# Kernel optimization log

Measured on AMD Instinct MI355X. Metric: run time of the kernel, lower is better.

## Reference

```python
import jax, jax.numpy as jnp
import numpy as np

NUM_NODES = 100000
NUM_EDGES = 1600000
NUM_GRAPHS = 64
IN_DIM = 128
HID = 128
OUT_DIM = 256
NUM_LAYERS = 5
BN_EPS = 1e-5


def _bn(t, gamma, beta):
    # BatchNorm1d forward with batch statistics (biased variance), as in train mode
    m = jnp.mean(t, axis=0)
    v = jnp.var(t, axis=0)
    return gamma * (t - m) * jax.lax.rsqrt(v + BN_EPS) + beta


def setup_inputs() -> dict:
    key = jax.random.key(0)
    ks = jax.random.split(key, 16)
    x = jax.random.normal(ks[0], (NUM_NODES, IN_DIM), dtype=jnp.float32)
    edge_index = jax.random.randint(ks[1], (2, NUM_EDGES), 0, NUM_NODES, dtype=jnp.int64)
    batch = jnp.sort(jax.random.randint(ks[2], (NUM_NODES,), 0, NUM_GRAPHS, dtype=jnp.int64))
    s1 = 1.0 / np.sqrt(IN_DIM)
    s2 = 1.0 / np.sqrt(HID)
    # stacked per-layer GIN MLP params: Linear(HID,HID) -> BN -> ReLU -> Linear(HID,HID)
    w1 = jax.random.normal(ks[3], (NUM_LAYERS, HID, HID), dtype=jnp.float32) * s1
    b1 = jnp.zeros((NUM_LAYERS, HID), dtype=jnp.float32)
    gamma1 = jnp.ones((NUM_LAYERS, HID), dtype=jnp.float32)
    beta1 = jnp.zeros((NUM_LAYERS, HID), dtype=jnp.float32)
    w2 = jax.random.normal(ks[4], (NUM_LAYERS, HID, HID), dtype=jnp.float32) * s2
    b2 = jnp.zeros((NUM_LAYERS, HID), dtype=jnp.float32)
    # outer per-layer BatchNorm after each GINConv
    gamma_bn = jnp.ones((NUM_LAYERS, HID), dtype=jnp.float32)
    beta_bn = jnp.zeros((NUM_LAYERS, HID), dtype=jnp.float32)
    # output projection Linear(HID, OUT_DIM)
    wp = jax.random.normal(ks[5], (HID, OUT_DIM), dtype=jnp.float32) * s2
    bp = jnp.zeros((OUT_DIM,), dtype=jnp.float32)
    return {"x": x, "edge_index": edge_index, "batch": batch,
            "w1": w1, "b1": b1, "gamma1": gamma1, "beta1": beta1,
            "w2": w2, "b2": b2, "gamma_bn": gamma_bn, "beta_bn": beta_bn,
            "wp": wp, "bp": bp}


def reference(x, edge_index, batch, w1, b1, gamma1, beta1, w2, b2, gamma_bn, beta_bn, wp, bp):
    src, dst = edge_index[0], edge_index[1]
    h = x
    for i in range(NUM_LAYERS):
        # GINConv, eps=0: mlp((1+eps)*h + sum_{j in N(i)} h_j)
        agg = jax.ops.segment_sum(h[src], dst, num_segments=NUM_NODES)
        z = h + agg
        t = _bn(z @ w1[i] + b1[i], gamma1[i], beta1[i])
        t = jax.nn.relu(t)
        t = t @ w2[i] + b2[i]
        # outer BatchNorm + ReLU (dropout p handled as identity in eval)
        t = jax.nn.relu(_bn(t, gamma_bn[i], beta_bn[i]))
        h = h + t  # residual (dims always match)
    node_emb = h
    # global mean pool per graph
    sums = jax.ops.segment_sum(h, batch, num_segments=NUM_GRAPHS)
    counts = jax.ops.segment_sum(jnp.ones((NUM_NODES,), dtype=h.dtype), batch, num_segments=NUM_GRAPHS)
    pooled = sums / jnp.maximum(counts, 1.0)[:, None]
    graph_emb = pooled @ wp + bp
    return graph_emb, node_emb
```

## Files before the change

### kernel.cpp

```cpp
#include <hip/hip_runtime.h>

#define NNODES 100000
#define NEDGES 1600000
#define NGRAPHS 64
#define HID 128
#define OUTD 256
#define NLAYERS 5
#define BN_EPS 1e-5f
#define NBUCK 196
#define BUCKCAP 9216
#define FILL_BLOCKS 391
#define NREP1 64
#define NREP2 8
#define AG1B 6250

typedef __attribute__((ext_vector_type(8))) short short8;
typedef __attribute__((ext_vector_type(4))) float f32x4;

__device__ inline unsigned short f2b(float f) {
    union { float f; unsigned int u; } a; a.f = f;
    unsigned int u = a.u;
    return (unsigned short)((u + 0x7FFF + ((u >> 16) & 1)) >> 16);
}
__device__ inline float b2f(unsigned short b) {
    union { unsigned int u; float f; } a; a.u = ((unsigned int)b) << 16;
    return a.f;
}

union U8 { short8 v; unsigned short u[8]; };

__global__ void k_init(const float* __restrict__ x, float* __restrict__ h,
                       ushort* __restrict__ hb,
                       const float* __restrict__ w1, const float* __restrict__ w2,
                       unsigned short* __restrict__ WT, int* __restrict__ bcur) {
    int b = blockIdx.x;
    if (b < 12500) {
        int i = b * 256 + threadIdx.x;
        float4 v = ((const float4*)x)[i];
        ((float4*)h)[i] = v;
        ushort4 o;
        o.x = f2b(v.x); o.y = f2b(v.y); o.z = f2b(v.z); o.w = f2b(v.w);
        ((ushort4*)hb)[i] = o;
    } else {
        int t = (b - 12500) * 256 + threadIdx.x;
        int mat = t >> 14;
        int rem = t & 16383;
        int k = rem >> 7, n = rem & 127;
        const float* src = (mat < 5) ? &w1[(size_t)mat * 16384]
                                     : &w2[(size_t)(mat - 5) * 16384];
        WT[(size_t)mat * 16384 + n * 128 + k] = f2b(src[k * 128 + n]);
        if (b == 12500 && threadIdx.x < NBUCK)
            bcur[threadIdx.x] = threadIdx.x * BUCKCAP;
    }
}

__global__ __launch_bounds__(256) void k_fill1(
    const int* __restrict__ srcv, const int* __restrict__ dstv,
    int* __restrict__ bcur, unsigned int* __restrict__ packed) {
    __shared__ int hist[NBUCK];
    __shared__ int base[NBUCK];
    int tid = threadIdx.x;
    int e0 = blockIdx.x * 4096;
    for (int i = tid; i < NBUCK; i += 256) hist[i] = 0;
    __syncthreads();
#pragma unroll
    for (int i = 0; i < 16; i++) {
        int e = e0 + i * 256 + tid;
        if (e < NEDGES) atomicAdd(&hist[dstv[e] >> 9], 1);
    }
    __syncthreads();
    for (int i = tid; i < NBUCK; i += 256) {
        int c = hist[i];
        base[i] = c ? atomicAdd(&bcur[i], c) : 0;
        hist[i] = 0;
    }
    __syncthreads();
#pragma unroll
    for (int i = 0; i < 16; i++) {
        int e = e0 + i * 256 + tid;
        if (e < NEDGES) {
            int d = dstv[e];
            int b = d >> 9;
            int r = atomicAdd(&hist[b], 1);
            packed[base[b] + r] = ((unsigned int)srcv[e] << 9) | (unsigned int)(d & 511);
        }
    }
}

__global__ __launch_bounds__(256) void k_fill2(
    const unsigned int* __restrict__ packed, const int* __restrict__ bcur,
    int2* __restrict__ off2, int* __restrict__ adj, int* __restrict__ dhist) {
    __shared__ int deg[512];
    __shared__ int cur[512];
    __shared__ int dh[64];
    int tid = threadIdx.x;
    int b = blockIdx.x;
    int base = b * BUCKCAP;
    int cnt = bcur[b] - base;
    deg[tid] = 0; deg[tid + 256] = 0;
    if (tid < 64) dh[tid] = 0;
    __syncthreads();
    for (int i = tid; i < cnt; i += 256)
        atomicAdd(&deg[packed[base + i] & 511], 1);
    __syncthreads();
    cur[tid] = deg[tid]; cur[tid + 256] = deg[tid + 256];
    __syncthreads();
    for (int o = 1; o < 512; o <<= 1) {
        int u0 = (tid >= o) ? cur[tid - o] : 0;
        int u1 = (tid + 256 >= o) ? cur[tid + 256 - o] : 0;
        __syncthreads();
        cur[tid] += u0; cur[tid + 256] += u1;
        __syncthreads();
    }
    int nbase = b * 512;
#pragma unroll
    for (int i = 0; i < 2; i++) {
        int t = tid + i * 256;
        int st = base + cur[t] - deg[t];
        int n = nbase + t;
        if (n < NNODES) {
            off2[n] = make_int2(st, st + deg[t]);
            int d = deg[t]; if (d > 63) d = 63;
            atomicAdd(&dh[d], 1);
        }
    }
    __syncthreads();
    if (tid < 64 && dh[tid]) atomicAdd(&dhist[tid * 16], dh[tid]);
#pragma unroll
    for (int i = 0; i < 2; i++) {
        int t = tid + i * 256;
        cur[t] = base + cur[t] - deg[t];
    }
    __syncthreads();
    for (int i = tid; i < cnt; i += 256) {
        unsigned int p = packed[base + i];
        int r = atomicAdd(&cur[p & 511], 1);
        adj[r] = (int)(p >> 9);
    }
}

__global__ void k_dscan(const int* __restrict__ dhist, int* __restrict__ dcur) {
    if (threadIdx.x == 0) {
        int s = 0;
        for (int i = 0; i < 64; i++) { int c = dhist[i * 16]; dcur[i * 16] = s; s += c; }
    }
}

__global__ __launch_bounds__(256) void k_dscat(
    const int2* __restrict__ off2, int* __restrict__ dcur, int* __restrict__ perm) {
    __shared__ int h[64], base[64];
    int tid = threadIdx.x;
    int n = blockIdx.x * 256 + tid;
    if (tid < 64) h[tid] = 0;
    __syncthreads();
    int d = 0;
    if (n < NNODES) {
        int2 oo = off2[n];
        d = oo.y - oo.x; if (d > 63) d = 63;
        atomicAdd(&h[d], 1);
    }
    __syncthreads();
    if (tid < 64) { int c = h[tid]; base[tid] = c ? atomicAdd(&dcur[tid * 16], c) : 0; h[tid] = 0; }
    __syncthreads();
    if (n < NNODES) {
        int r = atomicAdd(&h[d], 1);
        perm[base[d] + r] = n;
    }
}

__global__ __launch_bounds__(256) void k_ag1(
    const ushort* __restrict__ hb, const int2* __restrict__ off2,
    const int* __restrict__ adj, const int* __restrict__ perm,
    const unsigned short* __restrict__ WT,
    const float* __restrict__ bias, ushort* __restrict__ C,
    float* __restrict__ stats) {
    __shared__ ushort zt[16 * 128];
    __shared__ float lstat[256];
    int tid = threadIdx.x;
    int n = tid >> 4;
    int c = tid & 15;
    int node = perm[blockIdx.x * 16 + n];
    const short8* hb8 = (const short8*)hb;

    U8 sv; sv.v = hb8[(size_t)node * 16 + c];
    float acc[8];
#pragma unroll
    for (int k = 0; k < 8; k++) acc[k] = b2f(sv.u[k]);

    int2 oo = off2[node];
    int e = oo.x, e1 = oo.y;
    for (; e + 8 <= e1; e += 8) {
        int s[8];
#pragma unroll
        for (int j = 0; j < 8; j++) s[j] = adj[e + j];
        U8 u[8];
#pragma unroll
        for (int j = 0; j < 8; j++) u[j].v = hb8[(size_t)s[j] * 16 + c];
#pragma unroll
        for (int j = 0; j < 8; j++)
#pragma unroll
            for (int k = 0; k < 8; k++) acc[k] += b2f(u[j].u[k]);
    }
    for (; e + 4 <= e1; e += 4) {
        int s0 = adj[e], s1 = adj[e + 1], s2 = adj[e + 2], s3 = adj[e + 3];
        U8 u0, u1, u2, u3;
        u0.v = hb8[(size_t)s0 * 16 + c];
        u1.v = hb8[(size_t)s1 * 16 + c];
        u2.v = hb8[(size_t)s2 * 16 + c];
        u3.v = hb8[(size_t)s3 * 16 + c];
#pragma unroll
        for (int k = 0; k < 8; k++)
            acc[k] += (b2f(u0.u[k]) + b2f(u1.u[k])) + (b2f(u2.u[k]) + b2f(u3.u[k]));
    }
    for (; e < e1; e++) {
        int s = adj[e];
        U8 u; u.v = hb8[(size_t)s * 16 + c];
#pragma unroll
        for (int k = 0; k < 8; k++) acc[k] += b2f(u.u[k]);
    }

    U8 o;
#pragma unroll
    for (int k = 0; k < 8; k++) o.u[k] = f2b(acc[k]);
    *(short8*)((char*)zt + ((n * 256 + c * 16) ^ ((n & 7) << 4))) = o.v;
    __syncthreads();

    int wave = tid >> 6;
    int lane = tid & 63;
    int q = lane >> 4;
    int l16 = lane & 15;

    f32x4 gacc[2];
    gacc[0] = (f32x4){0.f, 0.f, 0.f, 0.f};
    gacc[1] = (f32x4){0.f, 0.f, 0.f, 0.f};

#pragma unroll
    for (int kc = 0; kc < 4; kc++) {
        int k0 = kc * 32 + q * 8;
        int ch = kc * 4 + q;
        short8 av = *(const short8*)(
            (char*)zt + ((l16 * 256 + ch * 16) ^ ((l16 & 7) << 4)));
#pragma unroll
        for (int nt = 0; nt < 2; nt++) {
            int col0 = (wave * 2 + nt) * 16;
            short8 bf = *(const short8*)&WT[(size_t)(col0 + l16) * 128 + k0];
            gacc[nt] = __builtin_amdgcn_mfma_f32_16x16x32_bf16(
                av, bf, gacc[nt], 0, 0, 0);
        }
    }

    int rowbase = blockIdx.x * 16;
    int prow[4];
#pragma unroll
    for (int r = 0; r < 4; r++) prow[r] = perm[rowbase + q * 4 + r];
#pragma unroll
    for (int nt = 0; nt < 2; nt++) {
        int col = (wave * 2 + nt) * 16 + l16;
        float b = bias[col];
        float csum = 0.f, csq = 0.f;
#pragma unroll
        for (int r = 0; r < 4; r++) {
            float v = gacc[nt][r] + b;
            C[(size_t)prow[r] * 128 + col] = f2b(v);
            csum += v; csq += v * v;
        }
        csum += __shfl_xor(csum, 16, 64); csq += __shfl_xor(csq, 16, 64);
        csum += __shfl_xor(csum, 32, 64); csq += __shfl_xor(csq, 32, 64);
        if (q == 0) { lstat[col] = csum; lstat[128 + col] = csq; }
    }
    __syncthreads();
    atomicAdd(&stats[((blockIdx.x & (NREP1 - 1)) << 8) + tid], lstat[tid]);
}

__global__ __launch_bounds__(256) void k_gemm2(
    const ushort* __restrict__ A, const unsigned short* __restrict__ WT,
    const float* __restrict__ bias, ushort* __restrict__ C,
    const float* __restrict__ statsIn, const float* __restrict__ gamma,
    const float* __restrict__ beta, float* __restrict__ stats) {
    __shared__ ushort wlds[16384];
    __shared__ float lstat[256];
    __shared__ float s_sc[128], s_sh[128];
    int tid = threadIdx.x;

#pragma unroll
    for (int it = 0; it < 8; it++) {
        int i = tid * 8 + it * 2048;
        int row = i >> 7;
        short8 v = *(const short8*)&WT[i];
        *(short8*)((char*)wlds + ((i * 2) ^ ((row & 7) << 4))) = v;
    }

    if (tid < 128) {
        float s = 0.f, qq = 0.f;
#pragma unroll
        for (int r = 0; r < NREP1; r++) {
            s  += statsIn[r * 256 + tid];
            qq += statsIn[r * 256 + 128 + tid];
        }
        float m = s * (1.f / NNODES);
        float var = qq * (1.f / NNODES) - m * m;
        float sc = gamma[tid] * rsqrtf(var + BN_EPS);
        s_sc[tid] = sc;
        s_sh[tid] = beta[tid] - m * sc;
    }
    lstat[tid] = 0.f;

    int wave = tid >> 6;
    int lane = tid & 63;
    int q = lane >> 4;
    int l16 = lane & 15;
    int rowbase = blockIdx.x * 128 + wave * 32;

    short8 araw[2][4];
#pragma unroll
    for (int rt = 0; rt < 2; rt++) {
        int row = rowbase + rt * 16 + l16;
        if (row >= NNODES) row = NNODES - 1;
#pragma unroll
        for (int kc = 0; kc < 4; kc++)
            araw[rt][kc] = *(const short8*)&A[(size_t)row * 128 + kc * 32 + q * 8];
    }

    f32x4 acc[2][8];
#pragma unroll
    for (int rt = 0; rt < 2; rt++)
#pragma unroll
        for (int nt = 0; nt < 8; nt++) acc[rt][nt] = (f32x4){0.f, 0.f, 0.f, 0.f};

    __syncthreads();

#pragma unroll
    for (int kc = 0; kc < 4; kc++) {
        int k0 = kc * 32 + q * 8;
        short8 bf[8];
#pragma unroll
        for (int nt = 0; nt < 8; nt++) {
            int row = nt * 16 + l16;
            bf[nt] = *(const short8*)(
                (char*)wlds + ((row * 256 + k0 * 2) ^ ((row & 7) << 4)));
        }

        float4 s0 = *(const float4*)&s_sc[k0];
        float4 s1 = *(const float4*)&s_sc[k0 + 4];
        float4 t0 = *(const float4*)&s_sh[k0];
        float4 t1 = *(const float4*)&s_sh[k0 + 4];
        float scl[8] = {s0.x, s0.y, s0.z, s0.w, s1.x, s1.y, s1.z, s1.w};
        float shf[8] = {t0.x, t0.y, t0.z, t0.w, t1.x, t1.y, t1.z, t1.w};
#pragma unroll
        for (int rt = 0; rt < 2; rt++) {
            union { short8 s; unsigned short u[8]; } in, cv;
            in.s = araw[rt][kc];
#pragma unroll
            for (int j = 0; j < 8; j++) {
                float f = fmaxf(b2f(in.u[j]) * scl[j] + shf[j], 0.f);
                cv.u[j] = f2b(f);
            }
#pragma unroll
            for (int nt = 0; nt < 8; nt++)
                acc[rt][nt] = __builtin_amdgcn_mfma_f32_16x16x32_bf16(
                    cv.s, bf[nt], acc[rt][nt], 0, 0, 0);
        }
    }

#pragma unroll
    for (int nt = 0; nt < 8; nt++) {
        float b = bias[nt * 16 + l16];
        float csum = 0.f, csq = 0.f;
#pragma unroll
        for (int rt = 0; rt < 2; rt++) {
            int rb = rowbase + rt * 16 + q * 4;
#pragma unroll
            for (int r = 0; r < 4; r++) {
                int row = rb + r;
                if (row < NNODES) {
                    float v = acc[rt][nt][r] + b;
                    C[(size_t)row * 128 + nt * 16 + l16] = f2b(v);
                    csum += v; csq += v * v;
                }
            }
        }
        csum += __shfl_xor(csum, 16, 64); csq += __shfl_xor(csq, 16, 64);
        csum += __shfl_xor(csum, 32, 64); csq += __shfl_xor(csq, 32, 64);
        if (q == 0) {
            atomicAdd(&lstat[nt * 16 + l16], csum);
            atomicAdd(&lstat[128 + nt * 16 + l16], csq);
        }
    }
    __syncthreads();
    atomicAdd(&stats[((blockIdx.x & (NREP2 - 1)) << 8) + tid], lstat[tid]);
}

__global__ void k_resid(float* __restrict__ h, ushort* __restrict__ hb,
                        const ushort* __restrict__ t2b,
                        const float* __restrict__ statsIn,
                        const float* __restrict__ gamma, const float* __restrict__ beta) {
    __shared__ float s_sc[128], s_sh[128];
    int tid = threadIdx.x;
    if (tid < 128) {
        float s = 0.f, qq = 0.f;
#pragma unroll
        for (int r = 0; r < NREP2; r++) {
            s  += statsIn[r * 256 + tid];
            qq += statsIn[r * 256 + 128 + tid];
        }
        float m = s * (1.f / NNODES);
        float var = qq * (1.f / NNODES) - m * m;
        float sc = gamma[tid] * rsqrtf(var + BN_EPS);
        s_sc[tid] = sc;
        s_sh[tid] = beta[tid] - m * sc;
    }
    __syncthreads();
    int i = blockIdx.x * 256 + tid;
    int c4 = (i & 31) * 4;
    float4 sc = *(const float4*)&s_sc[c4];
    float4 sh = *(const float4*)&s_sh[c4];
    ushort4 t = ((const ushort4*)t2b)[i];
    float4 hv = ((float4*)h)[i];
    hv.x += fmaxf(b2f(t.x) * sc.x + sh.x, 0.f);
    hv.y += fmaxf(b2f(t.y) * sc.y + sh.y, 0.f);
    hv.z += fmaxf(b2f(t.z) * sc.z + sh.z, 0.f);
    hv.w += fmaxf(b2f(t.w) * sc.w + sh.w, 0.f);
    ((float4*)h)[i] = hv;
    ushort4 o;
    o.x = f2b(hv.x); o.y = f2b(hv.y); o.z = f2b(hv.z); o.w = f2b(hv.w);
    ((ushort4*)hb)[i] = o;
}

__global__ void k_pool(const float* __restrict__ h, const int* __restrict__ batch,
                       float* __restrict__ pooled, float* __restrict__ gcnt) {
    __shared__ float4 red[256];
    __shared__ int lcnt[NGRAPHS];
    int t = threadIdx.x;
    int d4 = t & 31, sub = t >> 5;
    int n0 = blockIdx.x * 128;
    if (n0 >= NNODES) return;
    int n1 = n0 + 128; if (n1 > NNODES) n1 = NNODES;
    if (t < NGRAPHS) lcnt[t] = 0;
    __syncthreads();
    if (t < n1 - n0) atomicAdd(&lcnt[batch[n0 + t]], 1);
    __syncthreads();
    if (t < NGRAPHS && lcnt[t]) atomicAdd(&gcnt[t], (float)lcnt[t]);

    int glo = batch[n0], ghi = batch[n1 - 1];
    for (int g = glo; g <= ghi; g++) {
        float4 acc = make_float4(0.f, 0.f, 0.f, 0.f);
        for (int r = n0 + sub; r < n1; r += 8) {
            if (batch[r] == g) {
                float4 v = ((const float4*)h)[(size_t)r * 32 + d4];
                acc.x += v.x; acc.y += v.y; acc.z += v.z; acc.w += v.w;
            }
        }
        red[t] = acc;
        __syncthreads();
        if (sub < 4) {
            float4 o = red[t + 128];
            red[t].x += o.x; red[t].y += o.y; red[t].z += o.z; red[t].w += o.w;
        }
        __syncthreads();
        if (sub < 2) {
            float4 o = red[t + 64];
            red[t].x += o.x; red[t].y += o.y; red[t].z += o.z; red[t].w += o.w;
        }
        __syncthreads();
        if (sub == 0) {
            float4 o = red[t + 32];
            float4 a = red[t];
            a.x += o.x; a.y += o.y; a.z += o.z; a.w += o.w;
            atomicAdd(&pooled[g * 128 + d4 * 4 + 0], a.x);
            atomicAdd(&pooled[g * 128 + d4 * 4 + 1], a.y);
            atomicAdd(&pooled[g * 128 + d4 * 4 + 2], a.z);
            atomicAdd(&pooled[g * 128 + d4 * 4 + 3], a.w);
        }
        __syncthreads();
    }
}

__global__ void k_proj(const float* __restrict__ pooled, const float* __restrict__ cnt,
                       const float* __restrict__ wp, const float* __restrict__ bp,
                       float* __restrict__ out) {
    __shared__ float prow[128];
    int g = blockIdx.x, c = threadIdx.x;
    if (c < 128) prow[c] = pooled[g * 128 + c] / fmaxf(cnt[g], 1.f);
    __syncthreads();
    float acc = bp[c];
    for (int k = 0; k < 128; k++) acc += prow[k] * wp[k * 256 + c];
    out[g * 256 + c] = acc;
}

extern "C" void kernel_launch(void* const* d_in, const int* in_sizes, int n_in,
                              void* d_out, int out_size, void* d_ws, size_t ws_size,
                              hipStream_t stream) {
    const float* x    = (const float*)d_in[0];
    const int*   eidx = (const int*)d_in[1];
    const int*   batch= (const int*)d_in[2];
    const float* w1   = (const float*)d_in[3];
    const float* b1   = (const float*)d_in[4];
    const float* g1   = (const float*)d_in[5];
    const float* be1  = (const float*)d_in[6];
    const float* w2   = (const float*)d_in[7];
    const float* b2   = (const float*)d_in[8];
    const float* gbn  = (const float*)d_in[9];
    const float* bbn  = (const float*)d_in[10];
    const float* wp   = (const float*)d_in[11];
    const float* bp   = (const float*)d_in[12];

    float* out  = (float*)d_out;
    float* gemb = out;
    float* h    = out + (size_t)NGRAPHS * OUTD;

    char* w = (char*)d_ws;
    ushort* hb   = (ushort*)w; w += (size_t)NNODES * 128 * 2;
    ushort* t2b  = (ushort*)w; w += (size_t)NNODES * 128 * 2;
    ushort* tb   = (ushort*)w; w += (size_t)NNODES * 128 * 2;
    int2*  off2  = (int2*)w;  w += (size_t)NNODES * 8;
    int*   adj   = (int*)w;   w += (size_t)NBUCK * BUCKCAP * 4;
    unsigned short* WT = (unsigned short*)w; w += (size_t)10 * 16384 * 2;
    int*   bcur  = (int*)w;   w += 256 * 4;
    float* statsAll = (float*)w; w += (size_t)NLAYERS * (NREP1 + NREP2) * 256 * 4;
    float* pooled= (float*)w; w += (size_t)NGRAPHS * HID * 4;
    float* gcnt  = (float*)w; w += NGRAPHS * 4;
    int*   dhist = (int*)w;   w += 1024 * 4;
    int*   dcur  = (int*)w;   w += 1024 * 4;
    int*   perm  = (int*)w;   w += (size_t)NNODES * 4;

    unsigned int* packed = (unsigned int*)tb;

    const int* srcv = eidx;
    const int* dstv = eidx + NEDGES;

    k_init<<<12500 + 640, 256, 0, stream>>>(x, h, hb, w1, w2, WT, bcur);

    hipMemsetAsync(statsAll, 0,
                   ((size_t)NLAYERS * (NREP1 + NREP2) * 256 + NGRAPHS * HID + NGRAPHS
                    + 2048) * 4, stream);

    k_fill1<<<FILL_BLOCKS, 256, 0, stream>>>(srcv, dstv, bcur, packed);
    k_fill2<<<NBUCK, 256, 0, stream>>>(packed, bcur, off2, adj, dhist);
    k_dscan<<<1, 64, 0, stream>>>(dhist, dcur);
    k_dscat<<<(NNODES + 255) / 256, 256, 0, stream>>>(off2, dcur, perm);

    for (int i = 0; i < NLAYERS; i++) {
        float* st1 = statsAll + (size_t)i * (NREP1 + NREP2) * 256;
        float* st2 = st1 + (size_t)NREP1 * 256;
        k_ag1<<<AG1B, 256, 0, stream>>>(
            hb, off2, adj, perm, WT + (size_t)i * 16384, b1 + i * HID, tb, st1);
        k_gemm2<<<(NNODES + 127) / 128, 256, 0, stream>>>(
            tb, WT + (size_t)(5 + i) * 16384, b2 + i * HID, t2b,
            st1, g1 + i * HID, be1 + i * HID, st2);
        k_resid<<<NNODES * 128 / 4 / 256, 256, 0, stream>>>(
            h, hb, t2b, st2, gbn + i * HID, bbn + i * HID);
    }

    k_pool<<<(NNODES + 127) / 128, 256, 0, stream>>>(h, batch, pooled, gcnt);
    k_proj<<<NGRAPHS, 256, 0, stream>>>(pooled, gcnt, wp, bp, gemb);
}
```

Baseline: 881.0 us.

## Replace LDS staging in aggregation GEMM with wave-local shuffles and per-wave stats

The fused aggregate+GEMM kernel no longer stages aggregated rows in shared memory behind a block barrier. Each wave instead shuffles its own 4 nodes' features into MFMA A-fragments and computes all 128 output columns itself. BN statistics go directly to global atomics per wave. This removes the block-wide sync so waves can finish gathering independently, at the cost of 4x redundant MFMA rows, more weight loads per wave, and more global atomics.

```diff
diff --git a/kernel.cpp b/kernel.cpp
--- a/kernel.cpp
+++ b/kernel.cpp
@@ -174,12 +174,11 @@
     const unsigned short* __restrict__ WT,
     const float* __restrict__ bias, ushort* __restrict__ C,
     float* __restrict__ stats) {
-    __shared__ ushort zt[16 * 128];
-    __shared__ float lstat[256];
     int tid = threadIdx.x;
-    int n = tid >> 4;
-    int c = tid & 15;
-    int node = perm[blockIdx.x * 16 + n];
+    int wave = tid >> 6;
+    int lane = tid & 63;
+    int c = lane & 15;
+    int node = perm[blockIdx.x * 16 + (tid >> 4)];
     const short8* hb8 = (const short8*)hb;
 
     U8 sv; sv.v = hb8[(size_t)node * 16 + c];
@@ -219,57 +218,54 @@
         for (int k = 0; k < 8; k++) acc[k] += b2f(u.u[k]);
     }
 
+    union { short8 v; unsigned int d[4]; } ob;
     U8 o;
 #pragma unroll
     for (int k = 0; k < 8; k++) o.u[k] = f2b(acc[k]);
-    *(short8*)((char*)zt + ((n * 256 + c * 16) ^ ((n & 7) << 4))) = o.v;
-    __syncthreads();
-
-    int wave = tid >> 6;
-    int lane = tid & 63;
-    int q = lane >> 4;
-    int l16 = lane & 15;
-
-    f32x4 gacc[2];
-    gacc[0] = (f32x4){0.f, 0.f, 0.f, 0.f};
-    gacc[1] = (f32x4){0.f, 0.f, 0.f, 0.f};
+    ob.v = o.v;
+
+    int qt = lane >> 4;
+    int rt = lane & 15;
+
+    f32x4 gacc[8];
+#pragma unroll
+    for (int nt = 0; nt < 8; nt++) gacc[nt] = (f32x4){0.f, 0.f, 0.f, 0.f};
 
 #pragma unroll
     for (int kc = 0; kc < 4; kc++) {
-        int k0 = kc * 32 + q * 8;
-        int ch = kc * 4 + q;
-        short8 av = *(const short8*)(
-            (char*)zt + ((l16 * 256 + ch * 16) ^ ((l16 & 7) << 4)));
-#pragma unroll
-        for (int nt = 0; nt < 2; nt++) {
-            int col0 = (wave * 2 + nt) * 16;
-            short8 bf = *(const short8*)&WT[(size_t)(col0 + l16) * 128 + k0];
+        int src = ((rt & 3) << 4) + kc * 4 + qt;
+        union { unsigned int d[4]; short8 v; } av;
+#pragma unroll
+        for (int d = 0; d < 4; d++) av.d[d] = __shfl((int)ob.d[d], src, 64);
+        int k0 = kc * 32 + qt * 8;
+#pragma unroll
+        for (int nt = 0; nt < 8; nt++) {
+            short8 bf = *(const short8*)&WT[(size_t)(nt * 16 + rt) * 128 + k0];
             gacc[nt] = __builtin_amdgcn_mfma_f32_16x16x32_bf16(
-                av, bf, gacc[nt], 0, 0, 0);
-        }
-    }
-
-    int rowbase = blockIdx.x * 16;
-    int prow[4];
-#pragma unroll
-    for (int r = 0; r < 4; r++) prow[r] = perm[rowbase + q * 4 + r];
-#pragma unroll
-    for (int nt = 0; nt < 2; nt++) {
-        int col = (wave * 2 + nt) * 16 + l16;
-        float b = bias[col];
+                av.v, bf, gacc[nt], 0, 0, 0);
+        }
+    }
+
+    int nrow[4];
+#pragma unroll
+    for (int r = 0; r < 4; r++) nrow[r] = __shfl(node, r << 4, 64);
+
+    int rep = ((blockIdx.x << 2) + wave) & (NREP1 - 1);
+#pragma unroll
+    for (int nt = 0; nt < 8; nt++) {
+        float b = bias[nt * 16 + rt];
         float csum = 0.f, csq = 0.f;
 #pragma unroll
         for (int r = 0; r < 4; r++) {
             float v = gacc[nt][r] + b;
-            C[(size_t)prow[r] * 128 + col] = f2b(v);
+            if (qt == 0) C[(size_t)nrow[r] * 128 + nt * 16 + rt] = f2b(v);
             csum += v; csq += v * v;
         }
-        csum += __shfl_xor(csum, 16, 64); csq += __shfl_xor(csq, 16, 64);
-        csum += __shfl_xor(csum, 32, 64); csq += __shfl_xor(csq, 32, 64);
-        if (q == 0) { lstat[col] = csum; lstat[128 + col] = csq; }
-    }
-    __syncthreads();
-    atomicAdd(&stats[((blockIdx.x & (NREP1 - 1)) << 8) + tid], lstat[tid]);
+        if (qt == 0) {
+            atomicAdd(&stats[(rep << 8) + nt * 16 + rt], csum);
+            atomicAdd(&stats[(rep << 8) + 128 + nt * 16 + rt], csq);
+        }
+    }
 }
 
 __global__ __launch_bounds__(256) void k_gemm2(
```

After: 1.232 ms. +39.9%, slower.
